# Performance work log

Measured on AMD Instinct MI355X. Metric: run time of the kernel, lower is better.

## Reference

```python
import jax, jax.numpy as jnp
import numpy as np

N_NODES = 50000
N_EDGES = 800000
IN_DIM, HID_DIM, N_CLASS = 128, 128, 2
DROPOUT_P = 0.5
NEG_SLOPE = 0.01  # F.leaky_relu default


def gcn_conv(x, src, dst, W, b, n_nodes):
    """PyG GCNConv: add self-loops, sym-normalize, aggregate, then bias."""
    loops = jnp.arange(n_nodes, dtype=src.dtype)
    s = jnp.concatenate([src, loops])
    d = jnp.concatenate([dst, loops])
    # degree on A + I (edge weights = 1), counted at destination
    deg = jax.ops.segment_sum(jnp.ones_like(d, dtype=x.dtype), d, num_segments=n_nodes)
    dis = jnp.where(deg > 0, jax.lax.rsqrt(deg), 0.0)  # deg^{-1/2}
    norm = dis[s] * dis[d]                               # [E+N]
    h = x @ W                                            # [N, out]
    msg = h[s] * norm[:, None]                           # gather + scale
    out = jax.ops.segment_sum(msg, d, num_segments=n_nodes)  # scatter-add
    return out + b


def dropout(x, p, key):
    keep = 1.0 - p
    mask = jax.random.bernoulli(key, keep, x.shape)
    return jnp.where(mask, x / keep, 0.0)


def setup_inputs() -> dict:
    key = jax.random.key(0)
    ks = jax.random.split(key, 8)
    x = jax.random.normal(ks[0], (N_NODES, IN_DIM), dtype=jnp.float32)
    edge_index = jax.random.randint(ks[1], (2, N_EDGES), 0, N_NODES, dtype=jnp.int64)
    def glorot(k, fin, fout):
        lim = np.sqrt(6.0 / (fin + fout)).astype(np.float32)
        return jax.random.uniform(k, (fin, fout), jnp.float32, -lim, lim)
    W1 = glorot(ks[2], IN_DIM, HID_DIM)
    W2 = glorot(ks[3], HID_DIM, HID_DIM)
    W3 = glorot(ks[4], HID_DIM, N_CLASS)
    b1 = jnp.zeros((HID_DIM,), jnp.float32)
    b2 = jnp.zeros((HID_DIM,), jnp.float32)
    b3 = jnp.zeros((N_CLASS,), jnp.float32)
    return {"x": x, "edge_index": edge_index, "W1": W1, "b1": b1,
            "W2": W2, "b2": b2, "W3": W3, "b3": b3}


def reference(x, edge_index, W1, b1, W2, b2, W3, b3):
    src, dst = edge_index[0], edge_index[1]
    n = x.shape[0]
    dkey = jax.random.key(42)
    k1, k2 = jax.random.split(dkey)
    h = gcn_conv(x, src, dst, W1, b1, n)
    h = jax.nn.leaky_relu(h, NEG_SLOPE)
    h = dropout(h, DROPOUT_P, k1)
    h = gcn_conv(h, src, dst, W2, b2, n)
    h = jax.nn.leaky_relu(h, NEG_SLOPE)
    h = dropout(h, DROPOUT_P, k2)
    h = gcn_conv(h, src, dst, W3, b3, n)
    return jax.nn.log_softmax(h, axis=1)
```

## Files before the change

kernel.cpp:

```cpp
#include <hip/hip_runtime.h>
#include <stdint.h>

#define N_NODES 50000
#define N_EDGES 800000
#define DIM     128
#define TOT     (N_NODES * DIM)
#define NB   196
#define CHUNK 8192
#define NBLK 98
#define GCAP 4096
#define G3CAP 8192
#define XBLKS (TOT / 4 / 256)

typedef __attribute__((ext_vector_type(8))) unsigned short ushort8_t;
typedef __attribute__((ext_vector_type(8))) short bfrag;
typedef __attribute__((ext_vector_type(4))) float f32x4;

__host__ __device__ inline void threefry2x32(uint32_t k0, uint32_t k1,
                                             uint32_t x0, uint32_t x1,
                                             uint32_t& o0, uint32_t& o1) {
    uint32_t ks0 = k0, ks1 = k1, ks2 = k0 ^ k1 ^ 0x1BD11BDAu;
    uint32_t v0 = x0 + ks0, v1 = x1 + ks1;
#define TF_R(r) { v0 += v1; v1 = (v1 << (r)) | (v1 >> (32 - (r))); v1 ^= v0; }
    TF_R(13) TF_R(15) TF_R(26) TF_R(6)
    v0 += ks1; v1 += ks2 + 1u;
    TF_R(17) TF_R(29) TF_R(16) TF_R(24)
    v0 += ks2; v1 += ks0 + 2u;
    TF_R(13) TF_R(15) TF_R(26) TF_R(6)
    v0 += ks0; v1 += ks1 + 3u;
    TF_R(17) TF_R(29) TF_R(16) TF_R(24)
    v0 += ks1; v1 += ks2 + 4u;
    TF_R(13) TF_R(15) TF_R(26) TF_R(6)
    v0 += ks2; v1 += ks0 + 5u;
#undef TF_R
    o0 = v0; o1 = v1;
}

__device__ inline float drop_scale(uint32_t kk0, uint32_t kk1, uint32_t i) {
    uint32_t b0, b1;
    threefry2x32(kk0, kk1, 0u, i, b0, b1);
    uint32_t bits = b0 ^ b1;
    return (bits >> 31) ? 0.0f : 2.0f;
}

__device__ inline float bf2f(ushort u) {
    return __uint_as_float(((uint32_t)u) << 16);
}
__device__ inline float bfpair_lo(uint32_t u) { return __uint_as_float(u << 16); }
__device__ inline float bfpair_hi(uint32_t u) { return __uint_as_float(u & 0xffff0000u); }

__device__ inline ushort f2bf_rne(float f) {
    uint32_t bits = __float_as_uint(f);
    uint32_t lsb = (bits >> 16) & 1u;
    bits += 0x7fffu + lsb;
    return (ushort)(bits >> 16);
}

__global__ __launch_bounds__(256) void k_prep(const float* __restrict__ x,
                                              const float* __restrict__ W1,
                                              const float* __restrict__ W2,
                                              ushort* __restrict__ Xb,
                                              ushort* __restrict__ W1t,
                                              ushort* __restrict__ W2t,
                                              const int* __restrict__ dst,
                                              uint32_t* __restrict__ hist) {
    __shared__ uint32_t h[NB];
    int b = blockIdx.x;
    int t = threadIdx.x;
    if (b < XBLKS) {
        int i = b * 256 + t;
        float4 v = ((const float4*)x)[i];
        ushort4 o;
        o.x = f2bf_rne(v.x); o.y = f2bf_rne(v.y);
        o.z = f2bf_rne(v.z); o.w = f2bf_rne(v.w);
        ((ushort4*)Xb)[i] = o;
    } else if (b < XBLKS + 128) {
        int j = (b - XBLKS) * 256 + t;
        const float* W = (j < DIM * DIM) ? W1 : W2;
        ushort* Wt = (j < DIM * DIM) ? W1t : W2t;
        int i = j & (DIM * DIM - 1);
        int k = i >> 7, n = i & 127;
        Wt[n * DIM + k] = f2bf_rne(W[k * DIM + n]);
    } else {
        int hb = b - XBLKS - 128;
        if (t < NB) h[t] = 0u;
        __syncthreads();
        int base = hb * CHUNK;
        #pragma unroll
        for (int i = 0; i < CHUNK / 256; ++i) {
            int e = base + i * 256 + t;
            if (e < N_EDGES) atomicAdd(&h[((uint32_t)dst[e]) >> 8], 1u);
        }
        __syncthreads();
        if (t < NB) hist[(size_t)t * NBLK + hb] = h[t];
    }
}

__global__ void k_bscan(uint32_t* __restrict__ hist, uint32_t* __restrict__ bb) {
    __shared__ uint32_t cnt[256];
    int t = threadIdx.x;
    uint32_t running = 0;
    if (t < NB) {
        uint32_t* hp = hist + (size_t)t * NBLK;
        for (int blk = 0; blk < NBLK; ++blk) {
            uint32_t c = hp[blk];
            hp[blk] = running;
            running += c;
        }
    }
    cnt[t] = (t < NB) ? running : 0u;
    __syncthreads();
    for (int off = 1; off < 256; off <<= 1) {
        uint32_t x = (t >= off) ? cnt[t - off] : 0u;
        __syncthreads();
        cnt[t] += x;
        __syncthreads();
    }
    uint32_t incl = cnt[t];
    uint32_t base = incl - ((t < NB) ? running : 0u);
    if (t < NB) bb[t] = base;
    if (t == NB - 1) bb[NB] = incl;
    __syncthreads();
    if (t < NB) {
        uint32_t* hp = hist + (size_t)t * NBLK;
        for (int blk = 0; blk < NBLK; ++blk)
            hp[blk] += base;
    }
}

__global__ __launch_bounds__(256) void k_scatter(const int* __restrict__ src,
                                                 const int* __restrict__ dst,
                                                 const uint32_t* __restrict__ hist,
                                                 uint32_t* __restrict__ packed) {
    __shared__ uint32_t cur[NB];
    int t = threadIdx.x;
    int blk = blockIdx.x;
    if (t < NB) cur[t] = hist[(size_t)t * NBLK + blk];
    __syncthreads();
    int base = blk * CHUNK;
    #pragma unroll
    for (int i = 0; i < CHUNK / 256; ++i) {
        int e = base + i * 256 + t;
        if (e < N_EDGES) {
            uint32_t d = (uint32_t)dst[e];
            uint32_t s = (uint32_t)src[e];
            uint32_t b = d >> 8;
            uint32_t pos = atomicAdd(&cur[b], 1u);
            packed[pos] = ((d & 255u) << 16) | s;
        }
    }
}

__global__ __launch_bounds__(256) void k_fill(const uint32_t* __restrict__ bb,
                                              const uint32_t* __restrict__ packed,
                                              uint32_t* __restrict__ row,
                                              float* __restrict__ dis,
                                              ushort* __restrict__ col16) {
    __shared__ uint32_t sdeg[256];
    __shared__ uint32_t scan[256];
    __shared__ uint32_t cur[256];
    int b = blockIdx.x;
    int t = threadIdx.x;
    uint32_t base = bb[b], n = bb[b + 1] - base;
    sdeg[t] = 0u;
    __syncthreads();
    uint32_t mine[24]; int cnt = 0;
    for (uint32_t i = t; i < n; i += 256) {
        uint32_t u = packed[base + i];
        mine[cnt++] = u;
        atomicAdd(&sdeg[u >> 16], 1u);
    }
    __syncthreads();
    uint32_t myd = sdeg[t];
    scan[t] = myd;
    __syncthreads();
    for (int off = 1; off < 256; off <<= 1) {
        uint32_t x = (t >= off) ? scan[t - off] : 0u;
        __syncthreads();
        scan[t] += x;
        __syncthreads();
    }
    uint32_t excl = scan[t] - myd;
    cur[t] = excl;
    int v = b * 256 + t;
    if (v <= N_NODES) row[v] = base + excl;
    if (v < N_NODES)  dis[v] = 1.0f / sqrtf((float)(myd + 1u));
    __syncthreads();
    for (int j = 0; j < cnt; ++j) {
        uint32_t u = mine[j];
        uint32_t pos = base + atomicAdd(&cur[u >> 16], 1u);
        col16[pos] = (ushort)(u & 0xffffu);
    }
}

__global__ __launch_bounds__(256) void k_gemm_mfma(const ushort* __restrict__ Xb,
                                                   const ushort* __restrict__ Wt,
                                                   const float* __restrict__ dis,
                                                   ushort* __restrict__ Hb) {
    int tid = threadIdx.x;
    int w = tid >> 6, lane = tid & 63;
    int m0 = blockIdx.x * 128 + w * 32;
    int lrow = lane & 15, quad = lane >> 4;
    f32x4 acc[2][8] = {};
    for (int kt = 0; kt < DIM; kt += 32) {
        bfrag a[2], b[8];
        #pragma unroll
        for (int t = 0; t < 2; ++t) {
            int m = m0 + t * 16 + lrow;
            if (m >= N_NODES) m = 0;
            a[t] = *(const bfrag*)(Xb + (size_t)m * DIM + kt + quad * 8);
        }
        #pragma unroll
        for (int c = 0; c < 8; ++c) {
            int n = c * 16 + lrow;
            b[c] = *(const bfrag*)(Wt + (size_t)n * DIM + kt + quad * 8);
        }
        #pragma unroll
        for (int t = 0; t < 2; ++t)
            #pragma unroll
            for (int c = 0; c < 8; ++c)
                acc[t][c] = __builtin_amdgcn_mfma_f32_16x16x32_bf16(a[t], b[c], acc[t][c], 0, 0, 0);
    }
    #pragma unroll
    for (int t = 0; t < 2; ++t) {
        #pragma unroll
        for (int r = 0; r < 4; ++r) {
            int rowi = m0 + t * 16 + quad * 4 + r;
            if (rowi < N_NODES) {
                float dv = dis[rowi];
                #pragma unroll
                for (int c = 0; c < 8; ++c) {
                    int feat = c * 16 + lrow;
                    int fp = feat >> 5, off = feat & 31;
                    Hb[((size_t)fp * N_NODES + rowi) * 32 + off] = f2bf_rne(acc[t][c][r] * dv);
                }
            }
        }
    }
}

__global__ __launch_bounds__(256) void k_gather(const uint32_t* __restrict__ row,
                                                const ushort* __restrict__ col16,
                                                const float* __restrict__ dis,
                                                const ushort* __restrict__ Hb,
                                                const float* __restrict__ bias,
                                                ushort* __restrict__ OUTb,
                                                uint32_t kk0, uint32_t kk1) {
    __shared__ ushort scol[GCAP];
    __shared__ uint32_t srow[65];
    int fp = blockIdx.x & 3;
    int c = blockIdx.x >> 2;
    int tid = threadIdx.x;
    int nbase = c * 64;
    int nend = nbase + 64; if (nend > N_NODES) nend = N_NODES;
    int nloc = nend - nbase;
    for (int i = tid; i <= nloc; i += 256) srow[i] = row[nbase + i];
    __syncthreads();
    uint32_t eLo = srow[0];
    uint32_t count = srow[nloc] - eLo;
    bool staged = count <= GCAP;
    if (staged) {
        for (uint32_t i = tid; i < count; i += 256) scol[i] = col16[eLo + i];
    }
    __syncthreads();

    int nl = tid >> 2;
    int q  = tid & 3;
    int v = nbase + nl;
    if (v >= N_NODES) return;
    const ushort* Hf = Hb + (size_t)fp * N_NODES * 32;
    ushort8_t hv = *((const ushort8_t*)(Hf + (size_t)v * 32 + q * 8));
    float acc[8];
    #pragma unroll
    for (int j = 0; j < 8; ++j) acc[j] = bf2f(hv[j]);

    uint32_t e0 = srow[nl] - eLo, e1 = srow[nl + 1] - eLo;
    uint32_t e = e0;
    if (staged) {
        for (; e + 4 <= e1; e += 4) {
            uint32_t s0 = scol[e], s1 = scol[e + 1], s2 = scol[e + 2], s3 = scol[e + 3];
            ushort8_t h0 = *((const ushort8_t*)(Hf + (size_t)s0 * 32 + q * 8));
            ushort8_t h1 = *((const ushort8_t*)(Hf + (size_t)s1 * 32 + q * 8));
            ushort8_t h2 = *((const ushort8_t*)(Hf + (size_t)s2 * 32 + q * 8));
            ushort8_t h3 = *((const ushort8_t*)(Hf + (size_t)s3 * 32 + q * 8));
            #pragma unroll
            for (int j = 0; j < 8; ++j)
                acc[j] += (bf2f(h0[j]) + bf2f(h1[j])) + (bf2f(h2[j]) + bf2f(h3[j]));
        }
        for (; e < e1; ++e) {
            uint32_t s0 = scol[e];
            ushort8_t h0 = *((const ushort8_t*)(Hf + (size_t)s0 * 32 + q * 8));
            #pragma unroll
            for (int j = 0; j < 8; ++j) acc[j] += bf2f(h0[j]);
        }
    } else {
        for (; e < e1; ++e) {
            uint32_t s0 = col16[eLo + e];
            ushort8_t h0 = *((const ushort8_t*)(Hf + (size_t)s0 * 32 + q * 8));
            #pragma unroll
            for (int j = 0; j < 8; ++j) acc[j] += bf2f(h0[j]);
        }
    }

    float dv = dis[v];
    int cbase = fp * 32 + q * 8;
    uint32_t ibase = (uint32_t)(v * DIM + cbase);
    ushort8_t o;
    #pragma unroll
    for (int j = 0; j < 8; ++j) {
        float z = acc[j] * dv + bias[cbase + j];
        z = (z >= 0.f) ? z : 0.01f * z;
        z *= drop_scale(kk0, kk1, ibase + j);
        o[j] = f2bf_rne(z);
    }
    *((ushort8_t*)(OUTb + (size_t)v * DIM + cbase)) = o;
}

__global__ void k_gemm_cls(const ushort* __restrict__ Bb, const float* __restrict__ W3,
                           const float* __restrict__ dis, float* __restrict__ O) {
    int v = blockIdx.x * blockDim.x + threadIdx.x;
    if (v >= N_NODES) return;
    const uint32_t* r = (const uint32_t*)(Bb + (size_t)v * DIM);
    float a0 = 0.f, a1 = 0.f;
#pragma unroll 8
    for (int w = 0; w < 64; ++w) {
        uint32_t u = r[w];
        float x0 = bfpair_lo(u), x1 = bfpair_hi(u);
        const float* wp = W3 + w * 4;
        a0 += x0 * wp[0] + x1 * wp[2];
        a1 += x0 * wp[1] + x1 * wp[3];
    }
    float dv = dis[v];
    O[v * 2 + 0] = a0 * dv;
    O[v * 2 + 1] = a1 * dv;
}

__global__ __launch_bounds__(256) void k_gather3(const uint32_t* __restrict__ row,
                                                 const ushort* __restrict__ col16,
                                                 const float* __restrict__ dis,
                                                 const float* __restrict__ H3s,
                                                 const float* __restrict__ b3,
                                                 float* __restrict__ out) {
    __shared__ ushort scol[G3CAP];
    __shared__ uint32_t srow[257];
    int tid = threadIdx.x;
    int nbase = blockIdx.x * 256;
    int nend = nbase + 256; if (nend > N_NODES) nend = N_NODES;
    int nloc = nend - nbase;
    for (int i = tid; i <= nloc; i += 256) srow[i] = row[nbase + i];
    __syncthreads();
    uint32_t eLo = srow[0];
    uint32_t count = srow[nloc] - eLo;
    bool staged = count <= G3CAP;
    if (staged) {
        for (uint32_t i = tid; i < count; i += 256) scol[i] = col16[eLo + i];
    }
    __syncthreads();

    int v = nbase + tid;
    if (v >= N_NODES) return;
    const float2* H2 = (const float2*)H3s;
    float2 h = H2[v];
    float z0 = h.x, z1 = h.y;
    uint32_t e0 = srow[tid] - eLo, e1 = srow[tid + 1] - eLo;
    uint32_t e = e0;
    if (staged) {
        for (; e + 2 <= e1; e += 2) {
            float2 ha = H2[scol[e]];
            float2 hb = H2[scol[e + 1]];
            z0 += ha.x + hb.x; z1 += ha.y + hb.y;
        }
        if (e < e1) {
            float2 ha = H2[scol[e]];
            z0 += ha.x; z1 += ha.y;
        }
    } else {
        for (; e < e1; ++e) {
            float2 ha = H2[col16[eLo + e]];
            z0 += ha.x; z1 += ha.y;
        }
    }
    float dv = dis[v];
    z0 = z0 * dv + b3[0];
    z1 = z1 * dv + b3[1];
    float m = fmaxf(z0, z1);
    float lse = m + logf(expf(z0 - m) + expf(z1 - m));
    out[v * 2 + 0] = z0 - lse;
    out[v * 2 + 1] = z1 - lse;
}

extern "C" void kernel_launch(void* const* d_in, const int* in_sizes, int n_in,
                              void* d_out, int out_size, void* d_ws, size_t ws_size,
                              hipStream_t stream) {
    const float* x  = (const float*)d_in[0];
    const int*   ei = (const int*)d_in[1];
    const float* W1 = (const float*)d_in[2];
    const float* b1 = (const float*)d_in[3];
    const float* W2 = (const float*)d_in[4];
    const float* b2 = (const float*)d_in[5];
    const float* W3 = (const float*)d_in[6];
    const float* b3 = (const float*)d_in[7];
    float* out = (float*)d_out;

    const int* src = ei;
    const int* dst = ei + N_EDGES;

    uint32_t* wsu = (uint32_t*)d_ws;
    float*    wsf = (float*)d_ws;
    uint32_t* hist   = wsu;
    uint32_t* bb     = wsu + 19264;
    uint32_t* row    = wsu + 19584;
    float*    dis    = wsf + 69632;
    uint32_t* packed = wsu + 119680;
    ushort*   col16  = (ushort*)(wsu + 919680);
    ushort*   Hb     = (ushort*)(wsu + 1319680);
    ushort*   Xb     = (ushort*)(wsu + 4519680);
    ushort*   Bb     = (ushort*)(wsu + 7719680);
    ushort*   W1t    = (ushort*)(wsu + 10919680);
    ushort*   W2t    = (ushort*)(wsu + 10927872);
    float*    h3s    = wsf + 10936064;

    uint32_t k1a, k1b, k2a, k2b;
    threefry2x32(0u, 42u, 0u, 0u, k1a, k1b);
    threefry2x32(0u, 42u, 0u, 1u, k2a, k2b);

    k_prep<<<XBLKS + 128 + NBLK, 256, 0, stream>>>(x, W1, W2, Xb, W1t, W2t, dst, hist);
    k_bscan<<<1, 256, 0, stream>>>(hist, bb);
    k_scatter<<<NBLK, 256, 0, stream>>>(src, dst, hist, packed);
    k_fill<<<NB, 256, 0, stream>>>(bb, packed, row, dis, col16);

    int ggrid = ((N_NODES + 63) / 64) * 4;
    int mgrid = (N_NODES + 127) / 128;

    k_gemm_mfma<<<mgrid, 256, 0, stream>>>(Xb, W1t, dis, Hb);
    k_gather<<<ggrid, 256, 0, stream>>>(row, col16, dis, Hb, b1, Bb, k1a, k1b);

    k_gemm_mfma<<<mgrid, 256, 0, stream>>>(Bb, W2t, dis, Hb);
    k_gather<<<ggrid, 256, 0, stream>>>(row, col16, dis, Hb, b2, Bb, k2a, k2b);

    k_gemm_cls<<<(N_NODES + 255) / 256, 256, 0, stream>>>(Bb, W3, dis, h3s);
    k_gather3<<<(N_NODES + 255) / 256, 256, 0, stream>>>(row, col16, dis, h3s, b3, out);
}
```

Measured before the change: 254.9 us.

## Fuse CSR build stages and overlap first GEMM with bucket fill

Replaces the histogram, scan and scatter kernels with a single pass in k_prep. Each block reserves bucket space through global atomics into fixed-capacity bucket slots and also counts per-node degree with global atomics. A separate small kernel computes the normalisation from those degrees. The fill kernel now computes each bucket's base with a prefix scan over the bucket counts and shares its grid with the first GEMM, so the two run concurrently and fewer kernels are launched. Two costs come in exchange: roughly 800K global atomics on deg, and a fixed per-bucket capacity that silently drops edges on overflow. There is also a race, because the GEMM blocks read dis while the fill blocks in the same launch write it, though k_dis has already written the same values.

```diff
diff --git a/kernel.cpp b/kernel.cpp
--- a/kernel.cpp
+++ b/kernel.cpp
@@ -6,6 +6,7 @@
 #define DIM     128
 #define TOT     (N_NODES * DIM)
 #define NB   196
+#define CAP  8192
 #define CHUNK 8192
 #define NBLK 98
 #define GCAP 4096
@@ -56,14 +57,62 @@
     return (ushort)(bits >> 16);
 }
 
+__device__ inline void gemm_body(const ushort* __restrict__ Xb,
+                                 const ushort* __restrict__ Wt,
+                                 const float* __restrict__ dis,
+                                 ushort* __restrict__ Hb, int gb, int tid) {
+    int w = tid >> 6, lane = tid & 63;
+    int m0 = gb * 128 + w * 32;
+    int lrow = lane & 15, quad = lane >> 4;
+    f32x4 acc[2][8] = {};
+    for (int kt = 0; kt < DIM; kt += 32) {
+        bfrag a[2], b[8];
+        #pragma unroll
+        for (int t = 0; t < 2; ++t) {
+            int m = m0 + t * 16 + lrow;
+            if (m >= N_NODES) m = 0;
+            a[t] = *(const bfrag*)(Xb + (size_t)m * DIM + kt + quad * 8);
+        }
+        #pragma unroll
+        for (int c = 0; c < 8; ++c) {
+            int n = c * 16 + lrow;
+            b[c] = *(const bfrag*)(Wt + (size_t)n * DIM + kt + quad * 8);
+        }
+        #pragma unroll
+        for (int t = 0; t < 2; ++t)
+            #pragma unroll
+            for (int c = 0; c < 8; ++c)
+                acc[t][c] = __builtin_amdgcn_mfma_f32_16x16x32_bf16(a[t], b[c], acc[t][c], 0, 0, 0);
+    }
+    #pragma unroll
+    for (int t = 0; t < 2; ++t) {
+        #pragma unroll
+        for (int r = 0; r < 4; ++r) {
+            int rowi = m0 + t * 16 + quad * 4 + r;
+            if (rowi < N_NODES) {
+                float dv = dis[rowi];
+                #pragma unroll
+                for (int c = 0; c < 8; ++c) {
+                    int feat = c * 16 + lrow;
+                    int fp = feat >> 5, off = feat & 31;
+                    Hb[((size_t)fp * N_NODES + rowi) * 32 + off] = f2bf_rne(acc[t][c][r] * dv);
+                }
+            }
+        }
+    }
+}
+
 __global__ __launch_bounds__(256) void k_prep(const float* __restrict__ x,
                                               const float* __restrict__ W1,
                                               const float* __restrict__ W2,
                                               ushort* __restrict__ Xb,
                                               ushort* __restrict__ W1t,
                                               ushort* __restrict__ W2t,
+                                              const int* __restrict__ src,
                                               const int* __restrict__ dst,
-                                              uint32_t* __restrict__ hist) {
+                                              uint32_t* __restrict__ gcur,
+                                              uint32_t* __restrict__ deg,
+                                              uint32_t* __restrict__ packed) {
     __shared__ uint32_t h[NB];
     int b = blockIdx.x;
     int t = threadIdx.x;
@@ -82,91 +131,76 @@
         int k = i >> 7, n = i & 127;
         Wt[n * DIM + k] = f2bf_rne(W[k * DIM + n]);
     } else {
-        int hb = b - XBLKS - 128;
+        int sb = b - XBLKS - 128;
         if (t < NB) h[t] = 0u;
         __syncthreads();
-        int base = hb * CHUNK;
+        int base = sb * CHUNK;
         #pragma unroll
         for (int i = 0; i < CHUNK / 256; ++i) {
             int e = base + i * 256 + t;
             if (e < N_EDGES) atomicAdd(&h[((uint32_t)dst[e]) >> 8], 1u);
         }
         __syncthreads();
-        if (t < NB) hist[(size_t)t * NBLK + hb] = h[t];
-    }
-}
-
-__global__ void k_bscan(uint32_t* __restrict__ hist, uint32_t* __restrict__ bb) {
-    __shared__ uint32_t cnt[256];
-    int t = threadIdx.x;
-    uint32_t running = 0;
-    if (t < NB) {
-        uint32_t* hp = hist + (size_t)t * NBLK;
-        for (int blk = 0; blk < NBLK; ++blk) {
-            uint32_t c = hp[blk];
-            hp[blk] = running;
-            running += c;
-        }
-    }
-    cnt[t] = (t < NB) ? running : 0u;
-    __syncthreads();
-    for (int off = 1; off < 256; off <<= 1) {
-        uint32_t x = (t >= off) ? cnt[t - off] : 0u;
-        __syncthreads();
-        cnt[t] += x;
-        __syncthreads();
-    }
-    uint32_t incl = cnt[t];
-    uint32_t base = incl - ((t < NB) ? running : 0u);
-    if (t < NB) bb[t] = base;
-    if (t == NB - 1) bb[NB] = incl;
-    __syncthreads();
-    if (t < NB) {
-        uint32_t* hp = hist + (size_t)t * NBLK;
-        for (int blk = 0; blk < NBLK; ++blk)
-            hp[blk] += base;
-    }
-}
-
-__global__ __launch_bounds__(256) void k_scatter(const int* __restrict__ src,
-                                                 const int* __restrict__ dst,
-                                                 const uint32_t* __restrict__ hist,
-                                                 uint32_t* __restrict__ packed) {
-    __shared__ uint32_t cur[NB];
-    int t = threadIdx.x;
-    int blk = blockIdx.x;
-    if (t < NB) cur[t] = hist[(size_t)t * NBLK + blk];
-    __syncthreads();
-    int base = blk * CHUNK;
-    #pragma unroll
-    for (int i = 0; i < CHUNK / 256; ++i) {
-        int e = base + i * 256 + t;
-        if (e < N_EDGES) {
-            uint32_t d = (uint32_t)dst[e];
-            uint32_t s = (uint32_t)src[e];
-            uint32_t b = d >> 8;
-            uint32_t pos = atomicAdd(&cur[b], 1u);
-            packed[pos] = ((d & 255u) << 16) | s;
-        }
-    }
-}
-
-__global__ __launch_bounds__(256) void k_fill(const uint32_t* __restrict__ bb,
-                                              const uint32_t* __restrict__ packed,
-                                              uint32_t* __restrict__ row,
-                                              float* __restrict__ dis,
-                                              ushort* __restrict__ col16) {
+        if (t < NB) {
+            uint32_t c = h[t];
+            h[t] = c ? atomicAdd(&gcur[t], c) : 0u;
+        }
+        __syncthreads();
+        #pragma unroll
+        for (int i = 0; i < CHUNK / 256; ++i) {
+            int e = base + i * 256 + t;
+            if (e < N_EDGES) {
+                uint32_t d = (uint32_t)dst[e];
+                uint32_t s = (uint32_t)src[e];
+                uint32_t bk = d >> 8;
+                uint32_t pos = atomicAdd(&h[bk], 1u);
+                if (pos < CAP)
+                    packed[(size_t)bk * CAP + pos] = ((d & 255u) << 16) | s;
+                atomicAdd(&deg[d], 1u);
+            }
+        }
+    }
+}
+
+__global__ void k_dis(const uint32_t* __restrict__ deg, float* __restrict__ dis) {
+    int v = blockIdx.x * 256 + threadIdx.x;
+    if (v < N_NODES) dis[v] = 1.0f / sqrtf((float)(deg[v] + 1u));
+}
+
+__global__ __launch_bounds__(256) void k_fill_gemm(const uint32_t* __restrict__ gcur,
+                                                   const uint32_t* __restrict__ packed,
+                                                   uint32_t* __restrict__ row,
+                                                   float* __restrict__ dis,
+                                                   ushort* __restrict__ col16,
+                                                   const ushort* __restrict__ Xb,
+                                                   const ushort* __restrict__ W1t,
+                                                   ushort* __restrict__ Hb) {
     __shared__ uint32_t sdeg[256];
     __shared__ uint32_t scan[256];
     __shared__ uint32_t cur[256];
     int b = blockIdx.x;
     int t = threadIdx.x;
-    uint32_t base = bb[b], n = bb[b + 1] - base;
+    if (b >= NB) {
+        gemm_body(Xb, W1t, dis, Hb, b - NB, t);
+        return;
+    }
+    uint32_t n = gcur[b];
+    scan[t] = (t < b) ? gcur[t] : 0u;
+    __syncthreads();
+    for (int off = 1; off < 256; off <<= 1) {
+        uint32_t x = (t >= off) ? scan[t - off] : 0u;
+        __syncthreads();
+        scan[t] += x;
+        __syncthreads();
+    }
+    uint32_t cbase = scan[255];
+    __syncthreads();
+    uint32_t pbase = (uint32_t)b * CAP;
     sdeg[t] = 0u;
     __syncthreads();
     uint32_t mine[24]; int cnt = 0;
     for (uint32_t i = t; i < n; i += 256) {
-        uint32_t u = packed[base + i];
+        uint32_t u = packed[pbase + i];
         mine[cnt++] = u;
         atomicAdd(&sdeg[u >> 16], 1u);
     }
@@ -183,59 +217,13 @@
     uint32_t excl = scan[t] - myd;
     cur[t] = excl;
     int v = b * 256 + t;
-    if (v <= N_NODES) row[v] = base + excl;
+    if (v <= N_NODES) row[v] = cbase + excl;
     if (v < N_NODES)  dis[v] = 1.0f / sqrtf((float)(myd + 1u));
     __syncthreads();
     for (int j = 0; j < cnt; ++j) {
         uint32_t u = mine[j];
-        uint32_t pos = base + atomicAdd(&cur[u >> 16], 1u);
+        uint32_t pos = cbase + atomicAdd(&cur[u >> 16], 1u);
         col16[pos] = (ushort)(u & 0xffffu);
-    }
-}
-
-__global__ __launch_bounds__(256) void k_gemm_mfma(const ushort* __restrict__ Xb,
-                                                   const ushort* __restrict__ Wt,
-                                                   const float* __restrict__ dis,
-                                                   ushort* __restrict__ Hb) {
-    int tid = threadIdx.x;
-    int w = tid >> 6, lane = tid & 63;
-    int m0 = blockIdx.x * 128 + w * 32;
-    int lrow = lane & 15, quad = lane >> 4;
-    f32x4 acc[2][8] = {};
-    for (int kt = 0; kt < DIM; kt += 32) {
-        bfrag a[2], b[8];
-        #pragma unroll
-        for (int t = 0; t < 2; ++t) {
-            int m = m0 + t * 16 + lrow;
-            if (m >= N_NODES) m = 0;
-            a[t] = *(const bfrag*)(Xb + (size_t)m * DIM + kt + quad * 8);
-        }
-        #pragma unroll
-        for (int c = 0; c < 8; ++c) {
-            int n = c * 16 + lrow;
-            b[c] = *(const bfrag*)(Wt + (size_t)n * DIM + kt + quad * 8);
-        }
-        #pragma unroll
-        for (int t = 0; t < 2; ++t)
-            #pragma unroll
-            for (int c = 0; c < 8; ++c)
-                acc[t][c] = __builtin_amdgcn_mfma_f32_16x16x32_bf16(a[t], b[c], acc[t][c], 0, 0, 0);
-    }
-    #pragma unroll
-    for (int t = 0; t < 2; ++t) {
-        #pragma unroll
-        for (int r = 0; r < 4; ++r) {
-            int rowi = m0 + t * 16 + quad * 4 + r;
-            if (rowi < N_NODES) {
-                float dv = dis[rowi];
-                #pragma unroll
-                for (int c = 0; c < 8; ++c) {
-                    int feat = c * 16 + lrow;
-                    int fp = feat >> 5, off = feat & 31;
-                    Hb[((size_t)fp * N_NODES + rowi) * 32 + off] = f2bf_rne(acc[t][c][r] * dv);
-                }
-            }
-        }
     }
 }
 
@@ -316,6 +304,13 @@
     *((ushort8_t*)(OUTb + (size_t)v * DIM + cbase)) = o;
 }
 
+__global__ __launch_bounds__(256) void k_gemm_mfma(const ushort* __restrict__ Xb,
+                                                   const ushort* __restrict__ Wt,
+                                                   const float* __restrict__ dis,
+                                                   ushort* __restrict__ Hb) {
+    gemm_body(Xb, Wt, dis, Hb, blockIdx.x, threadIdx.x);
+}
+
 __global__ void k_gemm_cls(const ushort* __restrict__ Bb, const float* __restrict__ W3,
                            const float* __restrict__ dis, float* __restrict__ O) {
     int v = blockIdx.x * blockDim.x + threadIdx.x;
@@ -407,32 +402,36 @@
 
     uint32_t* wsu = (uint32_t*)d_ws;
     float*    wsf = (float*)d_ws;
-    uint32_t* hist   = wsu;
-    uint32_t* bb     = wsu + 19264;
-    uint32_t* row    = wsu + 19584;
-    float*    dis    = wsf + 69632;
-    uint32_t* packed = wsu + 119680;
-    ushort*   col16  = (ushort*)(wsu + 919680);
-    ushort*   Hb     = (ushort*)(wsu + 1319680);
-    ushort*   Xb     = (ushort*)(wsu + 4519680);
-    ushort*   Bb     = (ushort*)(wsu + 7719680);
-    ushort*   W1t    = (ushort*)(wsu + 10919680);
-    ushort*   W2t    = (ushort*)(wsu + 10927872);
-    float*    h3s    = wsf + 10936064;
+    uint32_t* gcur   = wsu;
+    uint32_t* deg    = wsu + 256;
+    uint32_t* row    = wsu + 50304;
+    float*    dis    = wsf + 100352;
+    uint32_t* packed = wsu + 150400;
+    ushort*   col16  = (ushort*)(wsu + 1756032);
+    ushort*   Hb     = (ushort*)(wsu + 2158848);
+    ushort*   Xb     = (ushort*)(wsu + 5358848);
+    ushort*   Bb     = (ushort*)(wsu + 8558848);
+    ushort*   W1t    = (ushort*)(wsu + 11758848);
+    ushort*   W2t    = (ushort*)(wsu + 11767040);
+    float*    h3s    = wsf + 11775232;
 
     uint32_t k1a, k1b, k2a, k2b;
     threefry2x32(0u, 42u, 0u, 0u, k1a, k1b);
     threefry2x32(0u, 42u, 0u, 1u, k2a, k2b);
 
-    k_prep<<<XBLKS + 128 + NBLK, 256, 0, stream>>>(x, W1, W2, Xb, W1t, W2t, dst, hist);
-    k_bscan<<<1, 256, 0, stream>>>(hist, bb);
-    k_scatter<<<NBLK, 256, 0, stream>>>(src, dst, hist, packed);
-    k_fill<<<NB, 256, 0, stream>>>(bb, packed, row, dis, col16);
-
+    hipMemsetAsync(gcur, 0, 256 * sizeof(uint32_t), stream);
+    hipMemsetAsync(deg, 0, N_NODES * sizeof(uint32_t), stream);
+
+    k_prep<<<XBLKS + 128 + NBLK, 256, 0, stream>>>(x, W1, W2, Xb, W1t, W2t,
+                                                   src, dst, gcur, deg, packed);
+    k_dis<<<(N_NODES + 255) / 256, 256, 0, stream>>>(deg, dis);
+
+    int mgrid = (N_NODES + 127) / 128;
     int ggrid = ((N_NODES + 63) / 64) * 4;
-    int mgrid = (N_NODES + 127) / 128;
-
-    k_gemm_mfma<<<mgrid, 256, 0, stream>>>(Xb, W1t, dis, Hb);
+
+    k_fill_gemm<<<NB + mgrid, 256, 0, stream>>>(gcur, packed, row, dis, col16,
+                                                Xb, W1t, Hb);
+
     k_gather<<<ggrid, 256, 0, stream>>>(row, col16, dis, Hb, b1, Bb, k1a, k1b);
 
     k_gemm_mfma<<<mgrid, 256, 0, stream>>>(Bb, W2t, dis, Hb);
```

After: 304.6 us. 1.2x slower.
